# Kernel optimization log

Measured on AMD Instinct MI355X. Metric: run time of the kernel, lower is better.

Reference implementation:

```python
import jax, jax.numpy as jnp
import numpy as np

B, N, DIN, DE, NH, DK = 4, 256, 128, 64, 8, 16


def setup_inputs() -> dict:
    key = jax.random.key(0)
    ks = jax.random.split(key, 8)
    s = 0.05
    return {
        "h": jax.random.normal(ks[0], (B, N, DIN), jnp.float32),
        "e": jax.random.normal(ks[1], (B, N, N, DE), jnp.float32),
        "mask": jnp.ones((B, N), jnp.float32),
        "WQ": jax.random.normal(ks[2], (DIN, NH * DK), jnp.float32) * s,
        "WK": jax.random.normal(ks[3], (DIN, NH * DK), jnp.float32) * s,
        "WV": jax.random.normal(ks[4], (DIN, NH * DK), jnp.float32) * s,
        "WE": jax.random.normal(ks[5], (DE, NH * DK), jnp.float32) * s,
        "WE2": jax.random.normal(ks[6], (DE, NH * DK), jnp.float32) * s,
    }


def reference(h, e, mask, WQ, WK, WV, WE, WE2):
    b, n, _ = h.shape
    Q = (h @ WQ).reshape(b, n, NH, DK)
    K = (h @ WK).reshape(b, n, NH, DK) * (float(DK) ** -0.5)
    V = (h @ WV).reshape(b, n, NH, DK)
    E = (e @ WE).reshape(b, n, n, NH, DK)
    E2 = (e @ WE2).reshape(b, n, n, NH, DK)
    # edge-augmented scores: (b, i, j, h, k)
    scores = jnp.einsum('bihk,bjhk->bijh', Q, K)[..., None] + E2
    scores = jnp.exp(jnp.clip(scores, -5.0, 5.0))
    attn_mask = mask[:, :, None, None, None] * mask[:, None, :, None, None]
    scores = scores * attn_mask
    softmax_denom = jnp.clip(scores.sum(axis=2), 1e-6, None)  # (b,i,h,k)
    scores = scores * attn_mask  # attn_dropout p=0.0 -> identity
    out = jnp.einsum('bijhk,bjhk->bihk', scores, V)
    out = out + (scores * E).sum(axis=2)
    out = out / softmax_denom
    return out.reshape(b, n, NH * DK)
```

## Files before the change

kernel.cpp:

```cpp
#include <hip/hip_runtime.h>

#define BB   4
#define NN   256
#define DIN  128
#define DE   64
#define NH   8
#define DK   16
#define CC   128

typedef __attribute__((ext_vector_type(8))) short short8;
typedef __attribute__((ext_vector_type(4))) float f32x4;

__device__ __forceinline__ unsigned short f2bfu(float f) {
    union { float f; unsigned int i; } v; v.f = f;
    unsigned int x = v.i;
    x += 0x7FFFu + ((x >> 16) & 1u);
    return (unsigned short)(x >> 16);
}

__global__ __launch_bounds__(256) void prep_kernel(
    const float* __restrict__ h, const float* __restrict__ WQ,
    const float* __restrict__ WK, const float* __restrict__ WV,
    const float* __restrict__ WE, const float* __restrict__ WE2,
    float* __restrict__ Qw, float* __restrict__ Kw, float* __restrict__ Vw,
    unsigned short* __restrict__ wfrag)
{
    __shared__ float hsh[4 * DIN];
    __shared__ float psum[4 * 1536];
    const int t = threadIdx.x;

    if (blockIdx.x >= 256) {
        const int tid  = (blockIdx.x - 256) * 256 + t;
        const int m    = tid >> 10;
        const int g    = (tid >> 7) & 7;
        const int ks   = (tid >> 6) & 1;
        const int lane = tid & 63;
        const int q4 = lane >> 4, l15 = lane & 15;
        const float* W = m ? WE2 : WE;
        union { uint4 u; unsigned short s[8]; } pk;
        #pragma unroll
        for (int ii = 0; ii < 8; ++ii) {
            const int d = ks * 32 + q4 * 8 + ii;
            pk.s[ii] = f2bfu(W[d * CC + g * 16 + l15]);
        }
        ((uint4*)wfrag)[tid] = pk.u;
        return;
    }

    const int r0 = blockIdx.x * 4;
    hsh[t]       = h[(size_t)r0 * DIN + t];
    hsh[256 + t] = h[(size_t)r0 * DIN + 256 + t];
    __syncthreads();

    const int cp  = t & 63;
    const int qtr = t >> 6;
    float aq[4][2], ak[4][2], av[4][2];
    #pragma unroll
    for (int r = 0; r < 4; ++r) {
        aq[r][0]=aq[r][1]=ak[r][0]=ak[r][1]=av[r][0]=av[r][1]=0.f;
    }
    #pragma unroll 4
    for (int dd = 0; dd < 32; ++dd) {
        const int d = qtr * 32 + dd;
        const float2 fq = ((const float2*)WQ)[d * 64 + cp];
        const float2 fk = ((const float2*)WK)[d * 64 + cp];
        const float2 fv = ((const float2*)WV)[d * 64 + cp];
        #pragma unroll
        for (int r = 0; r < 4; ++r) {
            const float hd = hsh[r * DIN + d];
            aq[r][0] = fmaf(hd, fq.x, aq[r][0]); aq[r][1] = fmaf(hd, fq.y, aq[r][1]);
            ak[r][0] = fmaf(hd, fk.x, ak[r][0]); ak[r][1] = fmaf(hd, fk.y, ak[r][1]);
            av[r][0] = fmaf(hd, fv.x, av[r][0]); av[r][1] = fmaf(hd, fv.y, av[r][1]);
        }
    }
    float* pq = psum + qtr * 1536;
    #pragma unroll
    for (int r = 0; r < 4; ++r) {
        pq[r*384       + 2*cp] = aq[r][0]; pq[r*384       + 2*cp+1] = aq[r][1];
        pq[r*384 + 128 + 2*cp] = ak[r][0]; pq[r*384 + 128 + 2*cp+1] = ak[r][1];
        pq[r*384 + 256 + 2*cp] = av[r][0]; pq[r*384 + 256 + 2*cp+1] = av[r][1];
    }
    __syncthreads();
    #pragma unroll
    for (int k = 0; k < 6; ++k) {
        const int o = k * 256 + t;
        float v = psum[o] + psum[1536 + o] + psum[3072 + o] + psum[4608 + o];
        const int r   = o / 384;
        const int mc  = o - r * 384;
        const int mat = mc >> 7;
        const int c   = mc & 127;
        const size_t idx = (size_t)(r0 + r) * CC + c;
        if      (mat == 0) Qw[idx] = v;
        else if (mat == 1) Kw[idx] = v * 0.25f;
        else               Vw[idx] = v;
    }
}

__global__ __launch_bounds__(512, 4) void attn_kernel(
    const float* __restrict__ e, const float* __restrict__ maskp,
    const unsigned short* __restrict__ wfrag,
    const float* __restrict__ Qw, const float* __restrict__ Kw,
    const float* __restrict__ Vw, float* __restrict__ out)
{
    __shared__ __align__(16) unsigned short esh[2][128 * DE];
    __shared__ float qk_sh[2][128 * 9];
    __shared__ float msk1_sh[2][NN];
    __shared__ float msk2_sh[2][NN];
    __shared__ __align__(16) float qrow_sh[2][CC];

    const int blk  = blockIdx.x;
    const int b    = blk >> 7;
    const int i0   = (blk & 127) * 2;
    const int t    = threadIdx.x;
    const int wave = t >> 6, lane = t & 63;
    const int q4   = lane >> 4;
    const int l15  = lane & 15;
    const int g    = wave;

    const int tr = t >> 8;
    const int tt = t & 255;

    const f32x4* erow = (const f32x4*)(e + (size_t)(b * NN + i0 + tr) * NN * DE);
    uint4* eshv = (uint4*)esh;

    f32x4 pf[4][2];
    #pragma unroll
    for (int it = 0; it < 4; ++it) {
        const int pp = it * 256 + tt;
        pf[it][0] = __builtin_nontemporal_load(&erow[2 * pp]);
        pf[it][1] = __builtin_nontemporal_load(&erow[2 * pp + 1]);
    }

    if (t < NN) {
        const float mj  = maskp[b * NN + t];
        const float mi0 = maskp[b * NN + i0];
        const float mi1 = maskp[b * NN + i0 + 1];
        const float a0 = mi0 * mj, a1 = mi1 * mj;
        msk1_sh[0][t] = a0;  msk2_sh[0][t] = a0 * a0;
        msk1_sh[1][t] = a1;  msk2_sh[1][t] = a1 * a1;
    }
    if (t < 256) {
        qrow_sh[t >> 7][t & 127] = Qw[(size_t)(b * NN + i0 + (t >> 7)) * CC + (t & 127)];
    }
    short8 bfragE[2], bfragS[2];
    {
        const uint4* wf = (const uint4*)wfrag;
        #pragma unroll
        for (int ks = 0; ks < 2; ++ks) {
            union { uint4 u; short8 s8; } cv;
            cv.u = wf[((0 * 8 + wave) * 2 + ks) * 64 + lane];
            bfragE[ks] = cv.s8;
            cv.u = wf[((1 * 8 + wave) * 2 + ks) * 64 + lane];
            bfragS[ks] = cv.s8;
        }
    }

#define EWRITE() {                                                             \
        _Pragma("unroll")                                                      \
        for (int it = 0; it < 4; ++it) {                                       \
            const int pp = it * 256 + tt;                                      \
            const int jl = pp >> 3, ch8 = pp & 7;                              \
            union { uint4 u; unsigned short s[8]; } pk;                        \
            pk.s[0]=f2bfu(pf[it][0][0]); pk.s[1]=f2bfu(pf[it][0][1]);          \
            pk.s[2]=f2bfu(pf[it][0][2]); pk.s[3]=f2bfu(pf[it][0][3]);          \
            pk.s[4]=f2bfu(pf[it][1][0]); pk.s[5]=f2bfu(pf[it][1][1]);          \
            pk.s[6]=f2bfu(pf[it][1][2]); pk.s[7]=f2bfu(pf[it][1][3]);          \
            eshv[tr * 1024 + jl * 8 + (ch8 ^ (jl & 7))] = pk.u;                \
        } }
    EWRITE();
    __syncthreads();

    #pragma unroll
    for (int it = 0; it < 4; ++it) {
        const int pp = it * 256 + tt;
        pf[it][0] = __builtin_nontemporal_load(&erow[2048 + 2 * pp]);
        pf[it][1] = __builtin_nontemporal_load(&erow[2048 + 2 * pp + 1]);
    }
    __builtin_amdgcn_sched_barrier(0);

    const float* vbase = Vw + ((size_t)(b * NN) + q4 * 4) * CC + g * 16 + l15;
    float vr[8][4];

#define QK_HALF(H) {                                                           \
        const int q = t & 31;                                                  \
        const int hq = q >> 2;                                                 \
        const float4 qv0 = ((const float4*)qrow_sh[0])[q];                     \
        const float4 qv1 = ((const float4*)qrow_sh[1])[q];                     \
        const float4* kb = (const float4*)(Kw + (size_t)(b * NN + (H)*128) * CC); \
        _Pragma("unroll 4")                                                    \
        for (int it = 0; it < 8; ++it) {                                       \
            const int c = it * 512 + t;                                        \
            const int jl = c >> 5;                                             \
            const float4 kv = kb[c];                                           \
            float p0 = kv.x*qv0.x + kv.y*qv0.y + kv.z*qv0.z + kv.w*qv0.w;      \
            float p1 = kv.x*qv1.x + kv.y*qv1.y + kv.z*qv1.z + kv.w*qv1.w;      \
            p0 += __shfl_xor(p0, 1); p0 += __shfl_xor(p0, 2);                  \
            p1 += __shfl_xor(p1, 1); p1 += __shfl_xor(p1, 2);                  \
            if ((t & 3) == 0) {                                                \
                qk_sh[0][jl * 9 + hq] = p0;                                    \
                qk_sh[1][jl * 9 + hq] = p1;                                    \
            }                                                                  \
        } }

#define VHOIST(H) {                                                            \
        _Pragma("unroll")                                                      \
        for (int s = 0; s < 8; ++s)                                            \
            _Pragma("unroll")                                                  \
            for (int r = 0; r < 4; ++r)                                        \
                vr[s][r] = vbase[((H)*128 + s * 16 + r) * CC];                 \
        }

    QK_HALF(0); VHOIST(0);
    __builtin_amdgcn_sched_barrier(0);
    __syncthreads();

    float acc[2] = {0.f, 0.f}, dnm[2] = {0.f, 0.f};
    const short8* ep = (const short8*)esh;

#define COMPUTE_HALF(H) {                                                      \
        _Pragma("unroll")                                                      \
        for (int s = 0; s < 8; ++s) {                                          \
            const int ja = s * 16 + l15;                                       \
            _Pragma("unroll")                                                  \
            for (int ri = 0; ri < 2; ++ri) {                                   \
                const short8 a0 = ep[ri*1024 + ja*8 + ((q4    ) ^ (ja & 7))];  \
                const short8 a1 = ep[ri*1024 + ja*8 + ((q4 + 4) ^ (ja & 7))];  \
                f32x4 s2 = {0.f,0.f,0.f,0.f}, eE = {0.f,0.f,0.f,0.f};          \
                s2 = __builtin_amdgcn_mfma_f32_16x16x32_bf16(a0, bfragS[0], s2, 0,0,0); \
                s2 = __builtin_amdgcn_mfma_f32_16x16x32_bf16(a1, bfragS[1], s2, 0,0,0); \
                eE = __builtin_amdgcn_mfma_f32_16x16x32_bf16(a0, bfragE[0], eE, 0,0,0); \
                eE = __builtin_amdgcn_mfma_f32_16x16x32_bf16(a1, bfragE[1], eE, 0,0,0); \
                _Pragma("unroll")                                              \
                for (int rq = 0; rq < 4; ++rq) {                               \
                    const int jl = s * 16 + q4 * 4 + rq;                       \
                    const int jg = (H) * 128 + jl;                             \
                    float sc = qk_sh[ri][jl * 9 + g] + s2[rq];                 \
                    sc = fminf(5.f, fmaxf(-5.f, sc));                          \
                    const float p = __expf(sc);                                \
                    dnm[ri] = fmaf(p, msk1_sh[ri][jg], dnm[ri]);               \
                    acc[ri] = fmaf(p * msk2_sh[ri][jg], vr[s][rq] + eE[rq], acc[ri]); \
                }                                                              \
            }                                                                  \
        } }

    COMPUTE_HALF(0);
    __syncthreads();

    EWRITE();
    __syncthreads();

    QK_HALF(1); VHOIST(1);
    __builtin_amdgcn_sched_barrier(0);
    __syncthreads();

    COMPUTE_HALF(1);

#undef COMPUTE_HALF
#undef VHOIST
#undef QK_HALF
#undef EWRITE

    #pragma unroll
    for (int ri = 0; ri < 2; ++ri) {
        float a = acc[ri], d = dnm[ri];
        a += __shfl_xor(a, 16); a += __shfl_xor(a, 32);
        d += __shfl_xor(d, 16); d += __shfl_xor(d, 32);
        if (lane < 16) {
            out[(size_t)(b * NN + i0 + ri) * CC + g * 16 + lane] =
                a / fmaxf(d, 1e-6f);
        }
    }
}

extern "C" void kernel_launch(void* const* d_in, const int* in_sizes, int n_in,
                              void* d_out, int out_size, void* d_ws, size_t ws_size,
                              hipStream_t stream)
{
    const float* h    = (const float*)d_in[0];
    const float* e    = (const float*)d_in[1];
    const float* mask = (const float*)d_in[2];
    const float* WQ   = (const float*)d_in[3];
    const float* WK   = (const float*)d_in[4];
    const float* WV   = (const float*)d_in[5];
    const float* WE   = (const float*)d_in[6];
    const float* WE2  = (const float*)d_in[7];

    unsigned short* wfrag = (unsigned short*)d_ws;
    float* Qw = (float*)((char*)d_ws + 32768);
    float* Kw = Qw + BB * NN * CC;
    float* Vw = Kw + BB * NN * CC;

    prep_kernel<<<264, 256, 0, stream>>>(h, WQ, WK, WV, WE, WE2,
                                         Qw, Kw, Vw, wfrag);
    attn_kernel<<<BB*NN/2, 512, 0, stream>>>(e, mask, wfrag, Qw, Kw, Vw,
                                             (float*)d_out);
}
```

Before: 166.6 us.

## Stage full e rows in LDS up front instead of double-buffered halves

The e tile for both query rows is now loaded, converted to bf16 and written into a shared buffer covering all 256 keys before compute starts. This replaces the two-phase scheme that prefetched the second half into registers while the first half was computed. The separate squared-mask shared array is dropped and m1*m1 is computed inline. LDS use doubles to about 64KB for e, which can cut occupancy, and the overlap of the second-half e load with first-half compute is lost, in exchange for fewer register-held prefetches and one fewer barrier phase.

```diff
diff --git a/kernel.cpp b/kernel.cpp
--- a/kernel.cpp
+++ b/kernel.cpp
@@ -102,10 +102,9 @@
     const float* __restrict__ Qw, const float* __restrict__ Kw,
     const float* __restrict__ Vw, float* __restrict__ out)
 {
-    __shared__ __align__(16) unsigned short esh[2][128 * DE];
+    __shared__ __align__(16) unsigned short esh[2][NN * DE];
     __shared__ float qk_sh[2][128 * 9];
     __shared__ float msk1_sh[2][NN];
-    __shared__ float msk2_sh[2][NN];
     __shared__ __align__(16) float qrow_sh[2][CC];
 
     const int blk  = blockIdx.x;
@@ -117,30 +116,44 @@
     const int l15  = lane & 15;
     const int g    = wave;
 
-    const int tr = t >> 8;
-    const int tt = t & 255;
-
-    const f32x4* erow = (const f32x4*)(e + (size_t)(b * NN + i0 + tr) * NN * DE);
-    uint4* eshv = (uint4*)esh;
-
-    f32x4 pf[4][2];
-    #pragma unroll
-    for (int it = 0; it < 4; ++it) {
-        const int pp = it * 256 + tt;
-        pf[it][0] = __builtin_nontemporal_load(&erow[2 * pp]);
-        pf[it][1] = __builtin_nontemporal_load(&erow[2 * pp + 1]);
+    {
+        uint4* eshv = (uint4*)esh;
+        const f32x4* er0 = (const f32x4*)(e + (size_t)(b * NN + i0)     * NN * DE);
+        const f32x4* er1 = (const f32x4*)(e + (size_t)(b * NN + i0 + 1) * NN * DE);
+        #pragma unroll
+        for (int it = 0; it < 4; ++it) {
+            const int pp = it * 512 + t;
+            const int jg = pp >> 3, ch = pp & 7;
+            const f32x4 f0 = __builtin_nontemporal_load(&er0[2 * pp]);
+            const f32x4 f1 = __builtin_nontemporal_load(&er0[2 * pp + 1]);
+            union { uint4 u; unsigned short s[8]; } pk;
+            pk.s[0]=f2bfu(f0[0]); pk.s[1]=f2bfu(f0[1]); pk.s[2]=f2bfu(f0[2]); pk.s[3]=f2bfu(f0[3]);
+            pk.s[4]=f2bfu(f1[0]); pk.s[5]=f2bfu(f1[1]); pk.s[6]=f2bfu(f1[2]); pk.s[7]=f2bfu(f1[3]);
+            eshv[jg * 8 + (ch ^ (jg & 7))] = pk.u;
+        }
+        #pragma unroll
+        for (int it = 0; it < 4; ++it) {
+            const int pp = it * 512 + t;
+            const int jg = pp >> 3, ch = pp & 7;
+            const f32x4 f0 = __builtin_nontemporal_load(&er1[2 * pp]);
+            const f32x4 f1 = __builtin_nontemporal_load(&er1[2 * pp + 1]);
+            union { uint4 u; unsigned short s[8]; } pk;
+            pk.s[0]=f2bfu(f0[0]); pk.s[1]=f2bfu(f0[1]); pk.s[2]=f2bfu(f0[2]); pk.s[3]=f2bfu(f0[3]);
+            pk.s[4]=f2bfu(f1[0]); pk.s[5]=f2bfu(f1[1]); pk.s[6]=f2bfu(f1[2]); pk.s[7]=f2bfu(f1[3]);
+            eshv[2048 + jg * 8 + (ch ^ (jg & 7))] = pk.u;
+        }
     }
 
     if (t < NN) {
         const float mj  = maskp[b * NN + t];
         const float mi0 = maskp[b * NN + i0];
         const float mi1 = maskp[b * NN + i0 + 1];
-        const float a0 = mi0 * mj, a1 = mi1 * mj;
-        msk1_sh[0][t] = a0;  msk2_sh[0][t] = a0 * a0;
-        msk1_sh[1][t] = a1;  msk2_sh[1][t] = a1 * a1;
+        msk1_sh[0][t] = mi0 * mj;
+        msk1_sh[1][t] = mi1 * mj;
     }
     if (t < 256) {
-        qrow_sh[t >> 7][t & 127] = Qw[(size_t)(b * NN + i0 + (t >> 7)) * CC + (t & 127)];
+        qrow_sh[t >> 7][t & 127] =
+            Qw[(size_t)(b * NN + i0 + (t >> 7)) * CC + (t & 127)];
     }
     short8 bfragE[2], bfragS[2];
     {
@@ -154,32 +167,12 @@
             bfragS[ks] = cv.s8;
         }
     }
-
-#define EWRITE() {                                                             \
-        _Pragma("unroll")                                                      \
-        for (int it = 0; it < 4; ++it) {                                       \
-            const int pp = it * 256 + tt;                                      \
-            const int jl = pp >> 3, ch8 = pp & 7;                              \
-            union { uint4 u; unsigned short s[8]; } pk;                        \
-            pk.s[0]=f2bfu(pf[it][0][0]); pk.s[1]=f2bfu(pf[it][0][1]);          \
-            pk.s[2]=f2bfu(pf[it][0][2]); pk.s[3]=f2bfu(pf[it][0][3]);          \
-            pk.s[4]=f2bfu(pf[it][1][0]); pk.s[5]=f2bfu(pf[it][1][1]);          \
-            pk.s[6]=f2bfu(pf[it][1][2]); pk.s[7]=f2bfu(pf[it][1][3]);          \
-            eshv[tr * 1024 + jl * 8 + (ch8 ^ (jl & 7))] = pk.u;                \
-        } }
-    EWRITE();
-    __syncthreads();
-
-    #pragma unroll
-    for (int it = 0; it < 4; ++it) {
-        const int pp = it * 256 + tt;
-        pf[it][0] = __builtin_nontemporal_load(&erow[2048 + 2 * pp]);
-        pf[it][1] = __builtin_nontemporal_load(&erow[2048 + 2 * pp + 1]);
-    }
-    __builtin_amdgcn_sched_barrier(0);
+    __syncthreads();
 
     const float* vbase = Vw + ((size_t)(b * NN) + q4 * 4) * CC + g * 16 + l15;
     float vr[8][4];
+    float acc[2] = {0.f, 0.f}, dnm[2] = {0.f, 0.f};
+    const short8* ep = (const short8*)esh;
 
 #define QK_HALF(H) {                                                           \
         const int q = t & 31;                                                  \
@@ -210,21 +203,14 @@
                 vr[s][r] = vbase[((H)*128 + s * 16 + r) * CC];                 \
         }
 
-    QK_HALF(0); VHOIST(0);
-    __builtin_amdgcn_sched_barrier(0);
-    __syncthreads();
-
-    float acc[2] = {0.f, 0.f}, dnm[2] = {0.f, 0.f};
-    const short8* ep = (const short8*)esh;
-
 #define COMPUTE_HALF(H) {                                                      \
         _Pragma("unroll")                                                      \
         for (int s = 0; s < 8; ++s) {                                          \
-            const int ja = s * 16 + l15;                                       \
+            const int jga = (H) * 128 + s * 16 + l15;        \
             _Pragma("unroll")                                                  \
             for (int ri = 0; ri < 2; ++ri) {                                   \
-                const short8 a0 = ep[ri*1024 + ja*8 + ((q4    ) ^ (ja & 7))];  \
-                const short8 a1 = ep[ri*1024 + ja*8 + ((q4 + 4) ^ (ja & 7))];  \
+                const short8 a0 = ep[ri*2048 + jga*8 + ((q4    ) ^ (jga & 7))];\
+                const short8 a1 = ep[ri*2048 + jga*8 + ((q4 + 4) ^ (jga & 7))];\
                 f32x4 s2 = {0.f,0.f,0.f,0.f}, eE = {0.f,0.f,0.f,0.f};          \
                 s2 = __builtin_amdgcn_mfma_f32_16x16x32_bf16(a0, bfragS[0], s2, 0,0,0); \
                 s2 = __builtin_amdgcn_mfma_f32_16x16x32_bf16(a1, bfragS[1], s2, 0,0,0); \
@@ -237,28 +223,27 @@
                     float sc = qk_sh[ri][jl * 9 + g] + s2[rq];                 \
                     sc = fminf(5.f, fmaxf(-5.f, sc));                          \
                     const float p = __expf(sc);                                \
-                    dnm[ri] = fmaf(p, msk1_sh[ri][jg], dnm[ri]);               \
-                    acc[ri] = fmaf(p * msk2_sh[ri][jg], vr[s][rq] + eE[rq], acc[ri]); \
+                    const float m1 = msk1_sh[ri][jg];                          \
+                    dnm[ri] = fmaf(p, m1, dnm[ri]);                            \
+                    acc[ri] = fmaf(p * (m1 * m1), vr[s][rq] + eE[rq], acc[ri]);\
                 }                                                              \
             }                                                                  \
         } }
 
+    QK_HALF(0); VHOIST(0);
+    __builtin_amdgcn_sched_barrier(0);
+    __syncthreads();
     COMPUTE_HALF(0);
-    __syncthreads();
-
-    EWRITE();
     __syncthreads();
 
     QK_HALF(1); VHOIST(1);
     __builtin_amdgcn_sched_barrier(0);
     __syncthreads();
-
     COMPUTE_HALF(1);
 
 #undef COMPUTE_HALF
 #undef VHOIST
 #undef QK_HALF
-#undef EWRITE
 
     #pragma unroll
     for (int ri = 0; ri < 2; ++ri) {
```

Result: faster. 161.5 us (-3.1%).
